# Optimization experiments

Hardware: AMD Instinct MI355X
Metric: run time of the kernel (lower is better)

The kernel has to match this reference:

```python
import jax, jax.numpy as jnp
import numpy as np

NUM_HEADS = 12

def setup_inputs() -> dict:
    key = jax.random.key(0)
    ks = jax.random.split(key, 6)
    B, N, C = 8, 1024, 768
    H = W = 32
    rel_sp_dim = 2 * H - 1  # 63
    head_dim = C // NUM_HEADS  # 64
    s = 0.02
    return {
        "x": jax.random.normal(ks[0], (B, N, C), dtype=jnp.float32),
        "qkv_w": jax.random.normal(ks[1], (3 * C, C), dtype=jnp.float32) * s,
        "rel_pos_h": jax.random.normal(ks[2], (rel_sp_dim, head_dim), dtype=jnp.float32) * s,
        "rel_pos_w": jax.random.normal(ks[3], (rel_sp_dim, head_dim), dtype=jnp.float32) * s,
        "proj_w": jax.random.normal(ks[4], (C, C), dtype=jnp.float32) * s,
        "proj_b": jax.random.normal(ks[5], (C,), dtype=jnp.float32) * s,
        "H": H,
        "W": W,
    }

def reference(x, qkv_w, rel_pos_h, rel_pos_w, proj_w, proj_b, H, W):
    B, N, C = x.shape
    nh = NUM_HEADS
    hd = C // nh
    scale = hd ** -0.5

    # QKV projection (no bias)
    qkv = (x @ qkv_w.T).reshape(B, N, 3, nh, hd)
    qkv = jnp.transpose(qkv, (2, 0, 3, 1, 4))  # [3, B, nh, N, hd]
    q, k, v = qkv[0] * scale, qkv[1], qkv[2]

    attn = jnp.einsum('bhqd,bhkd->bhqk', q, k)  # [B, nh, N, N]

    # relative position bias (q_shape == k_shape, so ratios are 1)
    dist_h = jnp.arange(H)[:, None] - jnp.arange(H)[None, :] + (H - 1)
    dist_w = jnp.arange(W)[:, None] - jnp.arange(W)[None, :] + (W - 1)
    Rh = rel_pos_h[dist_h]  # [H, H, hd]
    Rw = rel_pos_w[dist_w]  # [W, W, hd]

    r_q = q.reshape(B, nh, H, W, hd)
    rel_h = jnp.einsum('byhwc,hkc->byhwk', r_q, Rh)  # [B, nh, H, W, H]
    rel_w = jnp.einsum('byhwc,wkc->byhwk', r_q, Rw)  # [B, nh, H, W, W]

    attn = attn.reshape(B, nh, H, W, H, W)
    attn = attn + rel_h[:, :, :, :, :, None] + rel_w[:, :, :, :, None, :]
    attn = attn.reshape(B, nh, N, N)

    attn = jax.nn.softmax(attn, axis=-1)
    out = jnp.einsum('bhqk,bhkd->bhqd', attn, v)  # [B, nh, N, hd]
    out = jnp.transpose(out, (0, 2, 1, 3)).reshape(B, N, C)
    return out @ proj_w.T + proj_b
```

## Files before the change

### kernel.cpp

```cpp
#include <hip/hip_runtime.h>

#define DEVI __device__ __forceinline__

typedef float f32x4 __attribute__((ext_vector_type(4)));
typedef float f32x16 __attribute__((ext_vector_type(16)));
typedef short bf16x8 __attribute__((ext_vector_type(8)));
typedef unsigned int uint2v __attribute__((ext_vector_type(2)));

DEVI unsigned short f2bf(float f) {
  union { float f; unsigned int u; } v; v.f = f;
  unsigned int u = v.u;
  u += 0x7fffu + ((u >> 16) & 1u);
  return (unsigned short)(u >> 16);
}
DEVI float bf2f(unsigned short h) {
  union { unsigned int u; float f; } v; v.u = ((unsigned int)h) << 16;
  return v.f;
}

DEVI void gld_lds16(const void* g, void* l) {
  __builtin_amdgcn_global_load_lds(
      (const __attribute__((address_space(1))) void*)g,
      (__attribute__((address_space(3))) void*)l, 16, 0, 0);
}

DEVI unsigned int cvt_pk_bf16(float lo, float hi) {
  unsigned int r;
  asm("v_cvt_pk_bf16_f32 %0, %1, %2" : "=v"(r) : "v"(lo), "v"(hi));
  return r;
}

DEVI float exp2_raw(float x) {
  float r;
  asm("v_exp_f32 %0, %1" : "=v"(r) : "v"(x));
  return r;
}

#define MFMA16(a, b, c) __builtin_amdgcn_mfma_f32_16x16x32_bf16((a), (b), (c), 0, 0, 0)
#define MFMA32(a, b, c) __builtin_amdgcn_mfma_f32_32x32x16_bf16((a), (b), (c), 0, 0, 0)

#define QSCALE 0.18033688011112042f

__global__ void __launch_bounds__(256) convert3_kernel(
    const float* __restrict__ x, const float* __restrict__ qkv_w,
    const float* __restrict__ proj_w,
    unsigned short* __restrict__ xb, unsigned short* __restrict__ wqkv,
    unsigned short* __restrict__ wproj) {
  const int i = blockIdx.x * 256 + threadIdx.x;
  const float* src; unsigned short* dst; int off;
  if (i < 1572864)      { src = x;      dst = xb;    off = i; }
  else if (i < 2015232) { src = qkv_w;  dst = wqkv;  off = i - 1572864; }
  else                  { src = proj_w; dst = wproj; off = i - 2015232; }
  float4 v = ((const float4*)src)[off];
  ushort4 o;
  o.x = f2bf(v.x); o.y = f2bf(v.y); o.z = f2bf(v.z); o.w = f2bf(v.w);
  ((ushort4*)dst)[off] = o;
}

template <int MODE>
__global__ void __launch_bounds__(256) gemm_nt(
    const unsigned short* __restrict__ A,
    const unsigned short* __restrict__ Bw,
    unsigned short* __restrict__ oq,
    unsigned short* __restrict__ okk,
    unsigned short* __restrict__ ovt,
    float* __restrict__ of,
    const float* __restrict__ bias) {
  constexpr int K = 768;
  constexpr int NT = K / 64;
  const int tid = threadIdx.x;
  const int l = tid & 63, wv = tid >> 6;
  const int wy = wv >> 1, wx = wv & 1;
  const int lg = l >> 4, lr = l & 15;
  const int m0 = blockIdx.x * 128, n0 = blockIdx.y * 128;

  __shared__ __align__(16) unsigned short As[2][128 * 64];
  __shared__ __align__(16) unsigned short Bs[2][128 * 64];

  f32x4 acc[4][4] = {};

  auto stage = [&](int buf, int k0) {
#pragma unroll
    for (int c = 0; c < 4; ++c) {
      const int row = c * 32 + wv * 8 + (l >> 3);
      const int g = l & 7;
      const int off = ((g ^ (row & 7)) * 8);
      gld_lds16(A + (size_t)(m0 + row) * K + k0 + off, &As[buf][(c * 32 + wv * 8) * 64]);
      gld_lds16(Bw + (size_t)(n0 + row) * K + k0 + off, &Bs[buf][(c * 32 + wv * 8) * 64]);
    }
  };

  stage(0, 0);

  int cur = 0;
  for (int t = 0; t < NT; ++t) {
    if (t + 1 < NT) {
      stage(cur ^ 1, (t + 1) * 64);
      asm volatile("s_waitcnt vmcnt(8)" ::: "memory");
    } else {
      asm volatile("s_waitcnt vmcnt(0)" ::: "memory");
    }
    __builtin_amdgcn_s_barrier();
    __builtin_amdgcn_sched_barrier(0);

#pragma unroll
    for (int kk = 0; kk < 2; ++kk) {
      bf16x8 af[4], bfr[4];
#pragma unroll
      for (int i = 0; i < 4; ++i) {
        const int row = wy * 64 + i * 16 + lr;
        af[i] = *(const bf16x8*)&As[cur][row * 64 + (((kk * 4 + lg) ^ (row & 7)) * 8)];
      }
#pragma unroll
      for (int j = 0; j < 4; ++j) {
        const int row = wx * 64 + j * 16 + lr;
        bfr[j] = *(const bf16x8*)&Bs[cur][row * 64 + (((kk * 4 + lg) ^ (row & 7)) * 8)];
      }
#pragma unroll
      for (int i = 0; i < 4; ++i) {
#pragma unroll
        for (int j = 0; j < 4; ++j)
          acc[i][j] = MFMA16(af[i], bfr[j], acc[i][j]);
      }
    }

    asm volatile("s_waitcnt lgkmcnt(0)" ::: "memory");
    __builtin_amdgcn_sched_barrier(0);
    __builtin_amdgcn_s_barrier();
    cur ^= 1;
  }

  if constexpr (MODE == 0) {
    const int t = n0 / 768;
    if (t < 2) {
      unsigned short* base = (t == 0) ? oq : okk;
      const float sc = (t == 0) ? QSCALE : 1.0f;
#pragma unroll
      for (int i = 0; i < 4; ++i) {
        const int m = m0 + wy * 64 + i * 16 + lg * 4;
#pragma unroll
        for (int j = 0; j < 4; ++j) {
          const int col = n0 + wx * 64 + j * 16 + lr;
          const int rem = col - t * 768;
          const int h = rem >> 6, d = rem & 63;
#pragma unroll
          for (int r = 0; r < 4; ++r) {
            const int mm = m + r;
            const int b = mm >> 10, n = mm & 1023;
            base[(((size_t)(b * 12 + h) << 10) + n) * 64 + d] = f2bf(acc[i][j][r] * sc);
          }
        }
      }
    } else {
#pragma unroll
      for (int i = 0; i < 4; ++i) {
        const int m = m0 + wy * 64 + i * 16 + lg * 4;
        const int b = m >> 10, ntok = m & 1023;
#pragma unroll
        for (int j = 0; j < 4; ++j) {
          const int col = n0 + wx * 64 + j * 16 + lr;
          const int rem = col - 1536;
          const int h = rem >> 6, d = rem & 63;
          ushort4 pk4;
          pk4.x = f2bf(acc[i][j][0]); pk4.y = f2bf(acc[i][j][1]);
          pk4.z = f2bf(acc[i][j][2]); pk4.w = f2bf(acc[i][j][3]);
          *(ushort4*)(ovt + ((size_t)(b * 12 + h) * 64 + d) * 1024 + ntok) = pk4;
        }
      }
    }
  } else {
#pragma unroll
    for (int i = 0; i < 4; ++i) {
      const int m = m0 + wy * 64 + i * 16 + lg * 4;
#pragma unroll
      for (int j = 0; j < 4; ++j) {
        const int col = n0 + wx * 64 + j * 16 + lr;
        const float bv = bias[col];
#pragma unroll
        for (int r = 0; r < 4; ++r)
          of[(size_t)(m + r) * 768 + col] = acc[i][j][r] + bv;
      }
    }
  }
}

__global__ void __launch_bounds__(256) rel_kernel(
    const unsigned short* __restrict__ Q,
    const float* __restrict__ rph,
    const float* __restrict__ rpw,
    unsigned short* __restrict__ relh_t,
    unsigned short* __restrict__ relw_t) {
  const int bh = blockIdx.y;
  const int tid = threadIdx.x;
  const int l = tid & 63, w = tid >> 6;
  const int hi = l >> 5, l31 = l & 31;
  const int yx = blockIdx.x * 4 + w;

  const unsigned short* Qb = Q + (size_t)bh * 65536;

  f32x16 acch = {};
#pragma unroll
  for (int s4 = 0; s4 < 4; ++s4) {
    const float* ar = rph + (yx + 31 - l31) * 64 + s4 * 16 + hi * 8;
    float4 fa = ((const float4*)ar)[0], fb = ((const float4*)ar)[1];
    union { unsigned int u[4]; bf16x8 v; } au;
    au.u[0] = cvt_pk_bf16(fa.x, fa.y); au.u[1] = cvt_pk_bf16(fa.z, fa.w);
    au.u[2] = cvt_pk_bf16(fb.x, fb.y); au.u[3] = cvt_pk_bf16(fb.z, fb.w);
    bf16x8 qv = *(const bf16x8*)(Qb + (size_t)(yx * 32 + l31) * 64 + s4 * 16 + hi * 8);
    acch = MFMA32(au.v, qv, acch);
  }
  {
    unsigned short* ob = relh_t + (size_t)bh * 32768 + yx * 32 + l31;
#pragma unroll
    for (int r = 0; r < 16; ++r) {
      const int kh = (r & 3) + 8 * (r >> 2) + 4 * hi;
      ob[(size_t)kh * 1024] = f2bf(acch[r]);
    }
  }

  f32x16 accw = {};
#pragma unroll
  for (int s4 = 0; s4 < 4; ++s4) {
    const float* ar = rpw + (yx + 31 - l31) * 64 + s4 * 16 + hi * 8;
    float4 fa = ((const float4*)ar)[0], fb = ((const float4*)ar)[1];
    union { unsigned int u[4]; bf16x8 v; } au;
    au.u[0] = cvt_pk_bf16(fa.x, fa.y); au.u[1] = cvt_pk_bf16(fa.z, fa.w);
    au.u[2] = cvt_pk_bf16(fb.x, fb.y); au.u[3] = cvt_pk_bf16(fb.z, fb.w);
    bf16x8 qv = *(const bf16x8*)(Qb + (size_t)(l31 * 32 + yx) * 64 + s4 * 16 + hi * 8);
    accw = MFMA32(au.v, qv, accw);
  }
  {
    unsigned short* ob = relw_t + (size_t)bh * 32768 + l31 * 32 + yx;
#pragma unroll
    for (int r = 0; r < 16; ++r) {
      const int kw = (r & 3) + 8 * (r >> 2) + 4 * hi;
      ob[(size_t)kw * 1024] = f2bf(accw[r]);
    }
  }
}

__global__ void __launch_bounds__(256, 3) attn_kernel(
    const unsigned short* __restrict__ Q,
    const unsigned short* __restrict__ Km,
    const unsigned short* __restrict__ VT,
    const unsigned short* __restrict__ relh_t,
    const unsigned short* __restrict__ relw_t,
    unsigned short* __restrict__ out) {
  const int bid = blockIdx.x;
  const int qt = bid / 96;
  const int bh = bid % 96;
  const int q0 = qt * 128;
  const int tid = threadIdx.x;
  const int l = tid & 63, w = tid >> 6;
  const int hi = l >> 5, l31 = l & 31;

  __shared__ __align__(16) unsigned short Ks[2][64 * 64];
  __shared__ __align__(16) unsigned short VTs[2][64 * 64];
  __shared__ __align__(16) unsigned short rhsL[32 * 128];

  const unsigned short* Kb = Km + (size_t)bh * 65536;
  const unsigned short* Vb = VT + (size_t)bh * 65536;

#pragma unroll
  for (int c = 0; c < 2; ++c) {
    const int row = c * 16 + w * 4 + (l >> 4);
    gld_lds16(relh_t + (size_t)bh * 32768 + (size_t)row * 1024 + q0 + (l & 15) * 8,
              &rhsL[(c * 16 + w * 4) * 128]);
  }

  auto stage = [&](int buf, int t) {
#pragma unroll
    for (int c = 0; c < 2; ++c) {
      const int row = c * 32 + w * 8 + (l >> 3);
      const int g = l & 7;
      const int off = (g ^ (row & 7)) * 8;
      gld_lds16(Kb + (size_t)(t * 64 + row) * 64 + off, &Ks[buf][(c * 32 + w * 8) * 64]);
      gld_lds16(Vb + (size_t)row * 1024 + t * 64 + off, &VTs[buf][(c * 32 + w * 8) * 64]);
    }
  };

  bf16x8 qf[4];
  {
    const unsigned short* qp =
        Q + (size_t)bh * 65536 + (size_t)(q0 + w * 32 + l31) * 64 + hi * 8;
#pragma unroll
    for (int s4 = 0; s4 < 4; ++s4) qf[s4] = *(const bf16x8*)(qp + s4 * 16);
  }

  f32x16 rwacc;
  bf16x8 onesA;
  {
    bf16x8 idA0, idA1, rwB0, rwB1;
    const short onebf = (short)0x3F80;
#pragma unroll
    for (int e = 0; e < 8; ++e) {
      idA0[e] = (l31 == hi * 8 + e) ? onebf : (short)0;
      idA1[e] = (l31 == 16 + hi * 8 + e) ? onebf : (short)0;
      onesA[e] = onebf;
      rwB0[e] = (short)relw_t[(size_t)bh * 32768 + (size_t)(hi * 8 + e) * 1024 +
                              q0 + w * 32 + l31];
      rwB1[e] = (short)relw_t[(size_t)bh * 32768 + (size_t)(16 + hi * 8 + e) * 1024 +
                              q0 + w * 32 + l31];
    }
    f32x16 z = {};
    rwacc = MFMA32(idA0, rwB0, z);
    rwacc = MFMA32(idA1, rwB1, rwacc);
  }

  f32x16 od0 = {}, od1 = {}, sumacc = {};
  int cur = 0;

  stage(0, 0);

  for (int t = 0; t < 16; ++t) {
    if (t < 15) {
      stage(cur ^ 1, t + 1);
      asm volatile("s_waitcnt vmcnt(4)" ::: "memory");
    } else {
      asm volatile("s_waitcnt vmcnt(0)" ::: "memory");
    }
    __builtin_amdgcn_s_barrier();
    __builtin_amdgcn_sched_barrier(0);

    f32x16 s0, s1;
    __builtin_amdgcn_s_setprio(1);
    {
      const int row0 = l31, row1 = 32 + l31;
      bf16x8 kf0 = *(const bf16x8*)&Ks[cur][row0 * 64 + ((hi ^ (row0 & 7)) * 8)];
      bf16x8 kf1 = *(const bf16x8*)&Ks[cur][row1 * 64 + ((hi ^ (row1 & 7)) * 8)];
      s0 = MFMA32(kf0, qf[0], rwacc);
      s1 = MFMA32(kf1, qf[0], rwacc);
    }
#pragma unroll
    for (int s4 = 1; s4 < 4; ++s4) {
      {
        const int row = l31;
        bf16x8 kf = *(const bf16x8*)&Ks[cur][row * 64 + (((s4 * 2 + hi) ^ (row & 7)) * 8)];
        s0 = MFMA32(kf, qf[s4], s0);
      }
      {
        const int row = 32 + l31;
        bf16x8 kf = *(const bf16x8*)&Ks[cur][row * 64 + (((s4 * 2 + hi) ^ (row & 7)) * 8)];
        s1 = MFMA32(kf, qf[s4], s1);
      }
    }
    __builtin_amdgcn_s_setprio(0);

    const float rh0 = bf2f(rhsL[(2 * t) * 128 + w * 32 + l31]);
    const float rh1 = bf2f(rhsL[(2 * t + 1) * 128 + w * 32 + l31]);
#pragma unroll
    for (int r = 0; r < 16; ++r) {
      s0[r] = exp2_raw(s0[r] + rh0);
      s1[r] = exp2_raw(s1[r] + rh1);
    }

    bf16x8 pa[4];
#pragma unroll
    for (int ks = 0; ks < 4; ++ks) {
      unsigned int c0, c1, c2, c3;
      if (ks == 0) {
        c0 = cvt_pk_bf16(s0[0], s0[1]);  c1 = cvt_pk_bf16(s0[2], s0[3]);
        c2 = cvt_pk_bf16(s0[4], s0[5]);  c3 = cvt_pk_bf16(s0[6], s0[7]);
      } else if (ks == 1) {
        c0 = cvt_pk_bf16(s0[8], s0[9]);  c1 = cvt_pk_bf16(s0[10], s0[11]);
        c2 = cvt_pk_bf16(s0[12], s0[13]); c3 = cvt_pk_bf16(s0[14], s0[15]);
      } else if (ks == 2) {
        c0 = cvt_pk_bf16(s1[0], s1[1]);  c1 = cvt_pk_bf16(s1[2], s1[3]);
        c2 = cvt_pk_bf16(s1[4], s1[5]);  c3 = cvt_pk_bf16(s1[6], s1[7]);
      } else {
        c0 = cvt_pk_bf16(s1[8], s1[9]);  c1 = cvt_pk_bf16(s1[10], s1[11]);
        c2 = cvt_pk_bf16(s1[12], s1[13]); c3 = cvt_pk_bf16(s1[14], s1[15]);
      }
      uint2v x = __builtin_amdgcn_permlane32_swap(c0, c2, false, false);
      uint2v z = __builtin_amdgcn_permlane32_swap(c1, c3, false, false);
      union { unsigned int u[4]; bf16x8 v; } uu;
      uu.u[0] = x.x; uu.u[1] = z.x; uu.u[2] = x.y; uu.u[3] = z.y;
      pa[ks] = uu.v;
    }

    __builtin_amdgcn_s_setprio(1);
#pragma unroll
    for (int ks = 0; ks < 4; ++ks) {
      {
        const int row = l31;
        bf16x8 vf = *(const bf16x8*)&VTs[cur][row * 64 + (((ks * 2 + hi) ^ (row & 7)) * 8)];
        od0 = MFMA32(vf, pa[ks], od0);
      }
      {
        const int row = 32 + l31;
        bf16x8 vf = *(const bf16x8*)&VTs[cur][row * 64 + (((ks * 2 + hi) ^ (row & 7)) * 8)];
        od1 = MFMA32(vf, pa[ks], od1);
      }
      sumacc = MFMA32(onesA, pa[ks], sumacc);
    }
    __builtin_amdgcn_s_setprio(0);

    asm volatile("s_waitcnt lgkmcnt(0)" ::: "memory");
    __builtin_amdgcn_sched_barrier(0);
    __builtin_amdgcn_s_barrier();
    cur ^= 1;
  }

  const float inv = 1.f / sumacc[0];
  const int b = bh / 12, h = bh % 12;
  const int n = q0 + w * 32 + l31;
  unsigned short* ob = out + ((size_t)(b * 1024 + n)) * 768 + h * 64;
#pragma unroll
  for (int r4 = 0; r4 < 4; ++r4) {
    ushort4 p0, p1;
    p0.x = f2bf(od0[r4 * 4 + 0] * inv); p0.y = f2bf(od0[r4 * 4 + 1] * inv);
    p0.z = f2bf(od0[r4 * 4 + 2] * inv); p0.w = f2bf(od0[r4 * 4 + 3] * inv);
    p1.x = f2bf(od1[r4 * 4 + 0] * inv); p1.y = f2bf(od1[r4 * 4 + 1] * inv);
    p1.z = f2bf(od1[r4 * 4 + 2] * inv); p1.w = f2bf(od1[r4 * 4 + 3] * inv);
    *(ushort4*)(ob + 8 * r4 + 4 * hi) = p0;
    *(ushort4*)(ob + 32 + 8 * r4 + 4 * hi) = p1;
  }
}

extern "C" void kernel_launch(void* const* d_in, const int* in_sizes, int n_in,
                              void* d_out, int out_size, void* d_ws, size_t ws_size,
                              hipStream_t stream) {
  const float* x      = (const float*)d_in[0];
  const float* qkv_w  = (const float*)d_in[1];
  const float* rph    = (const float*)d_in[2];
  const float* rpw    = (const float*)d_in[3];
  const float* proj_w = (const float*)d_in[4];
  const float* proj_b = (const float*)d_in[5];
  float* out = (float*)d_out;

  char* ws = (char*)d_ws;
  unsigned short* xb     = (unsigned short*)(ws);
  unsigned short* wqkv   = (unsigned short*)(ws + 12582912);
  unsigned short* wproj  = (unsigned short*)(ws + 16121856);
  unsigned short* qb     = (unsigned short*)(ws + 17301504);
  unsigned short* kb     = (unsigned short*)(ws + 29884416);
  unsigned short* vbT    = (unsigned short*)(ws + 42467328);
  unsigned short* relh_t = (unsigned short*)(ws + 55050240);
  unsigned short* relw_t = (unsigned short*)(ws + 61341696);

  convert3_kernel<<<8448, 256, 0, stream>>>(x, qkv_w, proj_w, xb, wqkv, wproj);

  gemm_nt<0><<<dim3(64, 18), 256, 0, stream>>>(xb, wqkv, qb, kb, vbT, nullptr, nullptr);

  rel_kernel<<<dim3(8, 96), 256, 0, stream>>>(qb, rph, rpw, relh_t, relw_t);

  attn_kernel<<<768, 256, 0, stream>>>(qb, kb, vbT, relh_t, relw_t, xb);

  gemm_nt<1><<<dim3(64, 6), 256, 0, stream>>>(xb, wproj, nullptr, nullptr, nullptr, out, proj_b);
}
```

Baseline: 138.9 us.

## Give each attention wave two 32-row query tiles and sum softmax in registers

The attention kernel now runs 2 waves per block instead of 4, and each wave handles 64 query rows as two 32-row sub-tiles. Each K and V fragment read from LDS feeds two MFMAs, halving LDS reads per MFMA. The softmax denominator is now accumulated as a per-lane scalar sum plus a final permlane swap, replacing the ones-matrix MFMA. The cost is roughly double the accumulator registers, fewer waves per block for latency hiding, and each thread issuing twice as many staging loads.

New measurement: 149.9 us. +7.9%, slower.

```diff
diff --git a/kernel.cpp b/kernel.cpp
--- a/kernel.cpp
+++ b/kernel.cpp
@@ -239,7 +239,7 @@
   }
 }
 
-__global__ void __launch_bounds__(256, 3) attn_kernel(
+__global__ void __launch_bounds__(128, 2) attn_kernel(
     const unsigned short* __restrict__ Q,
     const unsigned short* __restrict__ Km,
     const unsigned short* __restrict__ VT,
@@ -262,52 +262,59 @@
   const unsigned short* Vb = VT + (size_t)bh * 65536;
 
 #pragma unroll
-  for (int c = 0; c < 2; ++c) {
-    const int row = c * 16 + w * 4 + (l >> 4);
+  for (int c = 0; c < 4; ++c) {
+    const int rowb = w * 16 + c * 4;
+    const int row = rowb + (l >> 4);
     gld_lds16(relh_t + (size_t)bh * 32768 + (size_t)row * 1024 + q0 + (l & 15) * 8,
-              &rhsL[(c * 16 + w * 4) * 128]);
+              &rhsL[rowb * 128]);
   }
 
   auto stage = [&](int buf, int t) {
 #pragma unroll
-    for (int c = 0; c < 2; ++c) {
-      const int row = c * 32 + w * 8 + (l >> 3);
+    for (int c = 0; c < 4; ++c) {
+      const int rowb = c * 16 + w * 8;
+      const int row = rowb + (l >> 3);
       const int g = l & 7;
       const int off = (g ^ (row & 7)) * 8;
-      gld_lds16(Kb + (size_t)(t * 64 + row) * 64 + off, &Ks[buf][(c * 32 + w * 8) * 64]);
-      gld_lds16(Vb + (size_t)row * 1024 + t * 64 + off, &VTs[buf][(c * 32 + w * 8) * 64]);
+      gld_lds16(Kb + (size_t)(t * 64 + row) * 64 + off, &Ks[buf][rowb * 64]);
+      gld_lds16(Vb + (size_t)row * 1024 + t * 64 + off, &VTs[buf][rowb * 64]);
     }
   };
 
-  bf16x8 qf[4];
+  bf16x8 qfA[4], qfB[4];
   {
     const unsigned short* qp =
-        Q + (size_t)bh * 65536 + (size_t)(q0 + w * 32 + l31) * 64 + hi * 8;
-#pragma unroll
-    for (int s4 = 0; s4 < 4; ++s4) qf[s4] = *(const bf16x8*)(qp + s4 * 16);
-  }
-
-  f32x16 rwacc;
-  bf16x8 onesA;
+        Q + (size_t)bh * 65536 + (size_t)(q0 + w * 64 + l31) * 64 + hi * 8;
+#pragma unroll
+    for (int s4 = 0; s4 < 4; ++s4) {
+      qfA[s4] = *(const bf16x8*)(qp + s4 * 16);
+      qfB[s4] = *(const bf16x8*)(qp + 32 * 64 + s4 * 16);
+    }
+  }
+
+  f32x16 rwaccA, rwaccB;
   {
-    bf16x8 idA0, idA1, rwB0, rwB1;
+    bf16x8 idA0, idA1, rwA0, rwA1, rwB0, rwB1;
     const short onebf = (short)0x3F80;
+    const size_t rwbase = (size_t)bh * 32768 + q0 + w * 64 + l31;
 #pragma unroll
     for (int e = 0; e < 8; ++e) {
       idA0[e] = (l31 == hi * 8 + e) ? onebf : (short)0;
       idA1[e] = (l31 == 16 + hi * 8 + e) ? onebf : (short)0;
-      onesA[e] = onebf;
-      rwB0[e] = (short)relw_t[(size_t)bh * 32768 + (size_t)(hi * 8 + e) * 1024 +
-                              q0 + w * 32 + l31];
-      rwB1[e] = (short)relw_t[(size_t)bh * 32768 + (size_t)(16 + hi * 8 + e) * 1024 +
-                              q0 + w * 32 + l31];
+      rwA0[e] = (short)relw_t[rwbase + (size_t)(hi * 8 + e) * 1024];
+      rwA1[e] = (short)relw_t[rwbase + (size_t)(16 + hi * 8 + e) * 1024];
+      rwB0[e] = (short)relw_t[rwbase + 32 + (size_t)(hi * 8 + e) * 1024];
+      rwB1[e] = (short)relw_t[rwbase + 32 + (size_t)(16 + hi * 8 + e) * 1024];
     }
     f32x16 z = {};
-    rwacc = MFMA32(idA0, rwB0, z);
-    rwacc = MFMA32(idA1, rwB1, rwacc);
-  }
-
-  f32x16 od0 = {}, od1 = {}, sumacc = {};
+    rwaccA = MFMA32(idA0, rwA0, z);
+    rwaccA = MFMA32(idA1, rwA1, rwaccA);
+    rwaccB = MFMA32(idA0, rwB0, z);
+    rwaccB = MFMA32(idA1, rwB1, rwaccB);
+  }
+
+  f32x16 odA0 = {}, odA1 = {}, odB0 = {}, odB1 = {};
+  float psumA = 0.f, psumB = 0.f;
   int cur = 0;
 
   stage(0, 0);
@@ -315,83 +322,94 @@
   for (int t = 0; t < 16; ++t) {
     if (t < 15) {
       stage(cur ^ 1, t + 1);
-      asm volatile("s_waitcnt vmcnt(4)" ::: "memory");
+      asm volatile("s_waitcnt vmcnt(8)" ::: "memory");
     } else {
       asm volatile("s_waitcnt vmcnt(0)" ::: "memory");
     }
     __builtin_amdgcn_s_barrier();
     __builtin_amdgcn_sched_barrier(0);
 
-    f32x16 s0, s1;
+    f32x16 sA0, sA1, sB0, sB1;
     __builtin_amdgcn_s_setprio(1);
     {
       const int row0 = l31, row1 = 32 + l31;
       bf16x8 kf0 = *(const bf16x8*)&Ks[cur][row0 * 64 + ((hi ^ (row0 & 7)) * 8)];
       bf16x8 kf1 = *(const bf16x8*)&Ks[cur][row1 * 64 + ((hi ^ (row1 & 7)) * 8)];
-      s0 = MFMA32(kf0, qf[0], rwacc);
-      s1 = MFMA32(kf1, qf[0], rwacc);
+      sA0 = MFMA32(kf0, qfA[0], rwaccA);
+      sA1 = MFMA32(kf1, qfA[0], rwaccA);
+      sB0 = MFMA32(kf0, qfB[0], rwaccB);
+      sB1 = MFMA32(kf1, qfB[0], rwaccB);
     }
 #pragma unroll
     for (int s4 = 1; s4 < 4; ++s4) {
-      {
-        const int row = l31;
-        bf16x8 kf = *(const bf16x8*)&Ks[cur][row * 64 + (((s4 * 2 + hi) ^ (row & 7)) * 8)];
-        s0 = MFMA32(kf, qf[s4], s0);
-      }
-      {
-        const int row = 32 + l31;
-        bf16x8 kf = *(const bf16x8*)&Ks[cur][row * 64 + (((s4 * 2 + hi) ^ (row & 7)) * 8)];
-        s1 = MFMA32(kf, qf[s4], s1);
-      }
+      const int row0 = l31, row1 = 32 + l31;
+      bf16x8 kf0 = *(const bf16x8*)&Ks[cur][row0 * 64 + (((s4 * 2 + hi) ^ (row0 & 7)) * 8)];
+      bf16x8 kf1 = *(const bf16x8*)&Ks[cur][row1 * 64 + (((s4 * 2 + hi) ^ (row1 & 7)) * 8)];
+      sA0 = MFMA32(kf0, qfA[s4], sA0);
+      sA1 = MFMA32(kf1, qfA[s4], sA1);
+      sB0 = MFMA32(kf0, qfB[s4], sB0);
+      sB1 = MFMA32(kf1, qfB[s4], sB1);
     }
     __builtin_amdgcn_s_setprio(0);
 
-    const float rh0 = bf2f(rhsL[(2 * t) * 128 + w * 32 + l31]);
-    const float rh1 = bf2f(rhsL[(2 * t + 1) * 128 + w * 32 + l31]);
+    const float rhA0 = bf2f(rhsL[(2 * t) * 128 + w * 64 + l31]);
+    const float rhB0 = bf2f(rhsL[(2 * t) * 128 + w * 64 + 32 + l31]);
+    const float rhA1 = bf2f(rhsL[(2 * t + 1) * 128 + w * 64 + l31]);
+    const float rhB1 = bf2f(rhsL[(2 * t + 1) * 128 + w * 64 + 32 + l31]);
 #pragma unroll
     for (int r = 0; r < 16; ++r) {
-      s0[r] = exp2_raw(s0[r] + rh0);
-      s1[r] = exp2_raw(s1[r] + rh1);
-    }
-
-    bf16x8 pa[4];
+      sA0[r] = exp2_raw(sA0[r] + rhA0); psumA += sA0[r];
+      sA1[r] = exp2_raw(sA1[r] + rhA1); psumA += sA1[r];
+      sB0[r] = exp2_raw(sB0[r] + rhB0); psumB += sB0[r];
+      sB1[r] = exp2_raw(sB1[r] + rhB1); psumB += sB1[r];
+    }
+
+    bf16x8 paA[4], paB[4];
 #pragma unroll
     for (int ks = 0; ks < 4; ++ks) {
-      unsigned int c0, c1, c2, c3;
+      unsigned int a0, a1, a2, a3, b0, b1, b2, b3;
       if (ks == 0) {
-        c0 = cvt_pk_bf16(s0[0], s0[1]);  c1 = cvt_pk_bf16(s0[2], s0[3]);
-        c2 = cvt_pk_bf16(s0[4], s0[5]);  c3 = cvt_pk_bf16(s0[6], s0[7]);
+        a0 = cvt_pk_bf16(sA0[0], sA0[1]);  a1 = cvt_pk_bf16(sA0[2], sA0[3]);
+        a2 = cvt_pk_bf16(sA0[4], sA0[5]);  a3 = cvt_pk_bf16(sA0[6], sA0[7]);
+        b0 = cvt_pk_bf16(sB0[0], sB0[1]);  b1 = cvt_pk_bf16(sB0[2], sB0[3]);
+        b2 = cvt_pk_bf16(sB0[4], sB0[5]);  b3 = cvt_pk_bf16(sB0[6], sB0[7]);
       } else if (ks == 1) {
-        c0 = cvt_pk_bf16(s0[8], s0[9]);  c1 = cvt_pk_bf16(s0[10], s0[11]);
-        c2 = cvt_pk_bf16(s0[12], s0[13]); c3 = cvt_pk_bf16(s0[14], s0[15]);
+        a0 = cvt_pk_bf16(sA0[8], sA0[9]);   a1 = cvt_pk_bf16(sA0[10], sA0[11]);
+        a2 = cvt_pk_bf16(sA0[12], sA0[13]); a3 = cvt_pk_bf16(sA0[14], sA0[15]);
+        b0 = cvt_pk_bf16(sB0[8], sB0[9]);   b1 = cvt_pk_bf16(sB0[10], sB0[11]);
+        b2 = cvt_pk_bf16(sB0[12], sB0[13]); b3 = cvt_pk_bf16(sB0[14], sB0[15]);
       } else if (ks == 2) {
-        c0 = cvt_pk_bf16(s1[0], s1[1]);  c1 = cvt_pk_bf16(s1[2], s1[3]);
-        c2 = cvt_pk_bf16(s1[4], s1[5]);  c3 = cvt_pk_bf16(s1[6], s1[7]);
+        a0 = cvt_pk_bf16(sA1[0], sA1[1]);  a1 = cvt_pk_bf16(sA1[2], sA1[3]);
+        a2 = cvt_pk_bf16(sA1[4], sA1[5]);  a3 = cvt_pk_bf16(sA1[6], sA1[7]);
+        b0 = cvt_pk_bf16(sB1[0], sB1[1]);  b1 = cvt_pk_bf16(sB1[2], sB1[3]);
+        b2 = cvt_pk_bf16(sB1[4], sB1[5]);  b3 = cvt_pk_bf16(sB1[6], sB1[7]);
       } else {
-        c0 = cvt_pk_bf16(s1[8], s1[9]);  c1 = cvt_pk_bf16(s1[10], s1[11]);
-        c2 = cvt_pk_bf16(s1[12], s1[13]); c3 = cvt_pk_bf16(s1[14], s1[15]);
-      }
-      uint2v x = __builtin_amdgcn_permlane32_swap(c0, c2, false, false);
-      uint2v z = __builtin_amdgcn_permlane32_swap(c1, c3, false, false);
-      union { unsigned int u[4]; bf16x8 v; } uu;
-      uu.u[0] = x.x; uu.u[1] = z.x; uu.u[2] = x.y; uu.u[3] = z.y;
-      pa[ks] = uu.v;
+        a0 = cvt_pk_bf16(sA1[8], sA1[9]);   a1 = cvt_pk_bf16(sA1[10], sA1[11]);
+        a2 = cvt_pk_bf16(sA1[12], sA1[13]); a3 = cvt_pk_bf16(sA1[14], sA1[15]);
+        b0 = cvt_pk_bf16(sB1[8], sB1[9]);   b1 = cvt_pk_bf16(sB1[10], sB1[11]);
+        b2 = cvt_pk_bf16(sB1[12], sB1[13]); b3 = cvt_pk_bf16(sB1[14], sB1[15]);
+      }
+      uint2v xa = __builtin_amdgcn_permlane32_swap(a0, a2, false, false);
+      uint2v za = __builtin_amdgcn_permlane32_swap(a1, a3, false, false);
+      uint2v xb2 = __builtin_amdgcn_permlane32_swap(b0, b2, false, false);
+      uint2v zb = __builtin_amdgcn_permlane32_swap(b1, b3, false, false);
+      union { unsigned int u[4]; bf16x8 v; } ua, ub;
+      ua.u[0] = xa.x; ua.u[1] = za.x; ua.u[2] = xa.y; ua.u[3] = za.y;
+      ub.u[0] = xb2.x; ub.u[1] = zb.x; ub.u[2] = xb2.y; ub.u[3] = zb.y;
+      paA[ks] = ua.v;
+      paB[ks] = ub.v;
     }
 
     __builtin_amdgcn_s_setprio(1);
 #pragma unroll
     for (int ks = 0; ks < 4; ++ks) {
-      {
-        const int row = l31;
-        bf16x8 vf = *(const bf16x8*)&VTs[cur][row * 64 + (((ks * 2 + hi) ^ (row & 7)) * 8)];
-        od0 = MFMA32(vf, pa[ks], od0);
-      }
-      {
-        const int row = 32 + l31;
-        bf16x8 vf = *(const bf16x8*)&VTs[cur][row * 64 + (((ks * 2 + hi) ^ (row & 7)) * 8)];
-        od1 = MFMA32(vf, pa[ks], od1);
-      }
-      sumacc = MFMA32(onesA, pa[ks], sumacc);
+      const int row0 = l31, row1 = 32 + l31;
+      bf16x8 vf0 = *(const bf16x8*)&VTs[cur][row0 * 64 + (((ks * 2 + hi) ^ (row0 & 7)) * 8)];
+      bf16x8 vf1 = *(const bf16x8*)&VTs[cur][row1 * 64 + (((ks * 2 + hi) ^ (row1 & 7)) * 8)];
+      odA0 = MFMA32(vf0, paA[ks], odA0);
+      odA1 = MFMA32(vf1, paA[ks], odA1);
+      odB0 = MFMA32(vf0, paB[ks], odB0);
+      odB1 = MFMA32(vf1, paB[ks], odB1);
     }
     __builtin_amdgcn_s_setprio(0);
 
@@ -401,19 +419,35 @@
     cur ^= 1;
   }
 
-  const float inv = 1.f / sumacc[0];
+  float sumA, sumB;
+  {
+    uint2v sw = __builtin_amdgcn_permlane32_swap(__float_as_uint(psumA),
+                                                 __float_as_uint(psumA), false, false);
+    sumA = __uint_as_float(sw.x) + __uint_as_float(sw.y);
+    uint2v sw2 = __builtin_amdgcn_permlane32_swap(__float_as_uint(psumB),
+                                                  __float_as_uint(psumB), false, false);
+    sumB = __uint_as_float(sw2.x) + __uint_as_float(sw2.y);
+  }
+  const float invA = 1.f / sumA, invB = 1.f / sumB;
   const int b = bh / 12, h = bh % 12;
-  const int n = q0 + w * 32 + l31;
-  unsigned short* ob = out + ((size_t)(b * 1024 + n)) * 768 + h * 64;
+  const int nA = q0 + w * 64 + l31;
+  unsigned short* obA = out + ((size_t)(b * 1024 + nA)) * 768 + h * 64;
+  unsigned short* obB = obA + (size_t)32 * 768;
 #pragma unroll
   for (int r4 = 0; r4 < 4; ++r4) {
-    ushort4 p0, p1;
-    p0.x = f2bf(od0[r4 * 4 + 0] * inv); p0.y = f2bf(od0[r4 * 4 + 1] * inv);
-    p0.z = f2bf(od0[r4 * 4 + 2] * inv); p0.w = f2bf(od0[r4 * 4 + 3] * inv);
-    p1.x = f2bf(od1[r4 * 4 + 0] * inv); p1.y = f2bf(od1[r4 * 4 + 1] * inv);
-    p1.z = f2bf(od1[r4 * 4 + 2] * inv); p1.w = f2bf(od1[r4 * 4 + 3] * inv);
-    *(ushort4*)(ob + 8 * r4 + 4 * hi) = p0;
-    *(ushort4*)(ob + 32 + 8 * r4 + 4 * hi) = p1;
+    ushort4 pA0, pA1, pB0, pB1;
+    pA0.x = f2bf(odA0[r4 * 4 + 0] * invA); pA0.y = f2bf(odA0[r4 * 4 + 1] * invA);
+    pA0.z = f2bf(odA0[r4 * 4 + 2] * invA); pA0.w = f2bf(odA0[r4 * 4 + 3] * invA);
+    pA1.x = f2bf(odA1[r4 * 4 + 0] * invA); pA1.y = f2bf(odA1[r4 * 4 + 1] * invA);
+    pA1.z = f2bf(odA1[r4 * 4 + 2] * invA); pA1.w = f2bf(odA1[r4 * 4 + 3] * invA);
+    pB0.x = f2bf(odB0[r4 * 4 + 0] * invB); pB0.y = f2bf(odB0[r4 * 4 + 1] * invB);
+    pB0.z = f2bf(odB0[r4 * 4 + 2] * invB); pB0.w = f2bf(odB0[r4 * 4 + 3] * invB);
+    pB1.x = f2bf(odB1[r4 * 4 + 0] * invB); pB1.y = f2bf(odB1[r4 * 4 + 1] * invB);
+    pB1.z = f2bf(odB1[r4 * 4 + 2] * invB); pB1.w = f2bf(odB1[r4 * 4 + 3] * invB);
+    *(ushort4*)(obA + 8 * r4 + 4 * hi) = pA0;
+    *(ushort4*)(obA + 32 + 8 * r4 + 4 * hi) = pA1;
+    *(ushort4*)(obB + 8 * r4 + 4 * hi) = pB0;
+    *(ushort4*)(obB + 32 + 8 * r4 + 4 * hi) = pB1;
   }
 }
 
@@ -444,7 +478,7 @@
 
   rel_kernel<<<dim3(8, 96), 256, 0, stream>>>(qb, rph, rpw, relh_t, relw_t);
 
-  attn_kernel<<<768, 256, 0, stream>>>(qb, kb, vbT, relh_t, relw_t, xb);
+  attn_kernel<<<768, 128, 0, stream>>>(qb, kb, vbT, relh_t, relw_t, xb);
 
   gemm_nt<1><<<dim3(64, 6), 256, 0, stream>>>(xb, wproj, nullptr, nullptr, nullptr, out, proj_b);
 }
```
